# Kernel tuning notes

Measured on AMD Instinct MI355X. Metric: run time of the kernel, lower is better.

Reference implementation:

```python
import jax, jax.numpy as jnp
import numpy as np

B, U, S, F, D = 4, 1024, 256, 16, 256
K_RED = 3          # fd_redundancy_k
MAX_STEPS = 32     # fixed trip count replacing the data-dependent while-loop
NEG = -1e9


def setup_inputs() -> dict:
    key = jax.random.key(0)
    ks = jax.random.split(key, 12)
    user_enc = jax.random.normal(ks[0], (B, U, D), dtype=jnp.float32)
    server_enc = jax.random.normal(ks[1], (B, S, D), dtype=jnp.float32)
    # small needs vs. generous capacities so the allocation loop runs many steps
    users = jax.random.uniform(ks[2], (B, U, 8), dtype=jnp.float32) * 0.1
    servers = jax.random.uniform(ks[3], (B, S, 8), dtype=jnp.float32) * 20.0 + 1.0
    connect = jax.random.uniform(ks[4], (B, U, S)) < 0.3
    fd_id = jax.random.randint(ks[5], (B, S), 0, F)
    fd_onehot = jax.nn.one_hot(fd_id, F, dtype=jnp.float32)
    W_state = jax.random.normal(ks[6], (D, 4), dtype=jnp.float32) * 0.5
    b_state = jnp.zeros((D,), dtype=jnp.float32)
    W_q = jax.random.normal(ks[7], (D, D), dtype=jnp.float32) * D ** -0.5
    W_k = jax.random.normal(ks[8], (D, D), dtype=jnp.float32) * D ** -0.5
    W_us = jax.random.normal(ks[9], (1, 3), dtype=jnp.float32) * 0.5
    return dict(user_enc=user_enc, server_enc=server_enc, users=users, servers=servers,
                connect=connect, fd_onehot=fd_onehot, W_state=W_state, b_state=b_state,
                W_q=W_q, W_k=W_k, W_us=W_us,
                fd_alpha=jnp.asarray(1.0, jnp.float32), fd_beta=jnp.asarray(0.0, jnp.float32),
                score_bias=jnp.asarray(0.0, jnp.float32))


def _forward(user_enc, server_enc, users, servers, connect, fd_onehot,
             W_state, b_state, W_q, W_k, W_us, fd_alpha, fd_beta, score_bias):
    b, u, _ = users.shape
    s = servers.shape[1]
    d = user_enc.shape[-1]
    needs = users[..., 2:6]            # [B,U,4]
    init_cap = servers[..., 3:7]       # [B,S,4]
    inv_sqrt_d = d ** -0.5
    kf = jnp.asarray(float(K_RED), jnp.float32)
    q = user_enc @ W_q.T               # [B,U,D]
    u_ids = jnp.arange(u)[None, :, None]   # [1,U,1]
    s_ids = jnp.arange(s)[None, None, :]   # [1,1,S]
    b_grid = jnp.broadcast_to(jnp.arange(b)[:, None], (b, s))

    def step(carry, _):
        cap, alloc, fd_seen, logp = carry
        rc = jnp.sum(alloc, axis=-1)                                   # [B,U]
        need_more = rc < K_RED
        can_fulfill = jnp.all(cap[:, None] >= needs[:, :, None], -1)   # [B,U,S]
        elig = connect & can_fulfill & need_more[:, :, None] & (~alloc)
        elig = elig & jnp.any(elig)                                    # freeze when done
        # fault-domain novelty score
        fd_overlap = jnp.einsum('buf,bsf->bus', fd_seen, fd_onehot)
        is_new_fd = (fd_overlap < 0.5).astype(jnp.float32)
        # capacity-conditioned server keys
        cap_ratio = cap / jnp.maximum(init_cap, 1e-6)
        k_vec = (server_enc + cap_ratio @ W_state.T + b_state) @ W_k.T
        logits = jnp.einsum('bud,bsd->bus', q, k_vec) * inv_sqrt_d + score_bias
        logits = logits + jnp.tanh(fd_alpha * is_new_fd + fd_beta)
        rc_f = rc.astype(jnp.float32)
        user_state = jnp.stack([rc_f / kf, jnp.clip(kf - rc_f, 0.0) / kf,
                                (rc == K_RED - 1).astype(jnp.float32)], axis=-1)
        logits = logits + user_state @ W_us.T                          # [B,U,1] bcast
        cand = jnp.where(elig, logits, NEG)
        valid_server = jnp.any(elig, axis=1)                           # [B,S]
        # each valid server proposes its best user (greedy policy)
        prop_u = jnp.argmax(cand, axis=1)                              # [B,S]
        logp_bs = jnp.max(cand, axis=1) - jax.scipy.special.logsumexp(cand, axis=1)
        prop_mask = valid_server[:, None, :] & (prop_u[:, None, :] == u_ids)  # [B,U,S]
        # each proposed user accepts its best proposing server
        chosen_s = jnp.argmax(jnp.where(prop_mask, logits, NEG), axis=-1)     # [B,U]
        has_prop = jnp.any(prop_mask, axis=-1)
        sel = has_prop[..., None] & (s_ids == chosen_s[..., None])     # [B,U,S]
        alloc = alloc | sel
        fd_contrib = jnp.where(valid_server[..., None], fd_onehot, 0.0)
        fd_seen = fd_seen.at[b_grid, prop_u].max(fd_contrib)
        used = jnp.einsum('bus,buc->bsc', sel.astype(jnp.float32), needs)
        cap = jnp.maximum(cap - used, 0.0)
        logp = logp + jnp.sum(jnp.where(prop_mask, logp_bs[:, None, :], 0.0), axis=-1)
        return (cap, alloc, fd_seen, logp), None

    init = (init_cap,
            jnp.zeros((b, u, s), dtype=bool),
            jnp.zeros((b, u, fd_onehot.shape[-1]), dtype=jnp.float32),
            jnp.zeros((b, u), dtype=jnp.float32))
    (cap, alloc, fd_seen, logp), _ = jax.lax.scan(step, init, None, length=MAX_STEPS)
    return logp.sum(axis=1), alloc, cap


def reference(user_enc, server_enc, users, servers, connect, fd_onehot,
              W_state, b_state, W_q, W_k, W_us, fd_alpha, fd_beta, score_bias):
    return _forward(user_enc, server_enc, users, servers, connect, fd_onehot,
                    W_state, b_state, W_q, W_k, W_us, fd_alpha, fd_beta, score_bias)
```

## Files before the change

### kernel.cpp

```cpp
#include <hip/hip_runtime.h>
#include <stdint.h>
#include <math.h>

#define NB 4
#define NU 1024
#define NS 256
#define NF 16
#define ND 256
#define NEGV -1000000000.0f
#define VBIT (1u << 14)
#define AGENT __HIP_MEMORY_SCOPE_AGENT
#define SPINCAP (1 << 20)
#define NGRP 64
#define SPB 4
#define NT 1024


__device__ __forceinline__ void gemm64_body(
    const float* __restrict__ A, const float* __restrict__ Bm, float* __restrict__ C,
    int K, int lda, int ldb, int ldc, const float* __restrict__ biasA, float alpha,
    int m0, int n0, int t,
    float (&As)[2][16][68], float (&Bs)[2][16][68]) {
  int tx = t & 15, ty = t >> 4;
  float acc[4][4];
#pragma unroll
  for (int i = 0; i < 4; i++)
#pragma unroll
    for (int j = 0; j < 4; j++) acc[i][j] = 0.f;
  int lr = t >> 2;
  int kq = (t & 3) * 4;
  {
    float4 av = *(const float4*)(A + (size_t)(m0 + lr) * lda + kq);
    if (biasA) {
      const float* bp = biasA + kq;
      av.x += bp[0]; av.y += bp[1]; av.z += bp[2]; av.w += bp[3];
    }
    As[0][kq + 0][lr] = av.x; As[0][kq + 1][lr] = av.y;
    As[0][kq + 2][lr] = av.z; As[0][kq + 3][lr] = av.w;
    float4 bv = *(const float4*)(Bm + (size_t)(n0 + lr) * ldb + kq);
    Bs[0][kq + 0][lr] = bv.x; Bs[0][kq + 1][lr] = bv.y;
    Bs[0][kq + 2][lr] = bv.z; Bs[0][kq + 3][lr] = bv.w;
  }
  __syncthreads();
  int nt = K >> 4;
  for (int ti = 0; ti < nt; ++ti) {
    int buf = ti & 1;
    float4 av2, bv2;
    bool more = (ti + 1 < nt);
    if (more) {
      int k0 = (ti + 1) << 4;
      av2 = *(const float4*)(A + (size_t)(m0 + lr) * lda + k0 + kq);
      if (biasA) {
        const float* bp = biasA + k0 + kq;
        av2.x += bp[0]; av2.y += bp[1]; av2.z += bp[2]; av2.w += bp[3];
      }
      bv2 = *(const float4*)(Bm + (size_t)(n0 + lr) * ldb + k0 + kq);
    }
#pragma unroll
    for (int k = 0; k < 16; ++k) {
      float4 a = *(const float4*)&As[buf][k][ty * 4];
      float4 bb = *(const float4*)&Bs[buf][k][tx * 4];
      float am[4] = {a.x, a.y, a.z, a.w};
      float bn[4] = {bb.x, bb.y, bb.z, bb.w};
#pragma unroll
      for (int i = 0; i < 4; ++i)
#pragma unroll
        for (int j = 0; j < 4; ++j) acc[i][j] += am[i] * bn[j];
    }
    if (more) {
      __syncthreads();
      int nb = buf ^ 1;
      As[nb][kq + 0][lr] = av2.x; As[nb][kq + 1][lr] = av2.y;
      As[nb][kq + 2][lr] = av2.z; As[nb][kq + 3][lr] = av2.w;
      Bs[nb][kq + 0][lr] = bv2.x; Bs[nb][kq + 1][lr] = bv2.y;
      Bs[nb][kq + 2][lr] = bv2.z; Bs[nb][kq + 3][lr] = bv2.w;
      __syncthreads();
    }
  }
#pragma unroll
  for (int i = 0; i < 4; ++i) {
    float4 o = make_float4(acc[i][0] * alpha, acc[i][1] * alpha,
                           acc[i][2] * alpha, acc[i][3] * alpha);
    *(float4*)(C + (size_t)(m0 + ty * 4 + i) * ldc + n0 + tx * 4) = o;
  }
}

__global__ __launch_bounds__(256) void k_pre1(
    const uint8_t* __restrict__ conn, const float* __restrict__ W_state,
    const float* __restrict__ W_k, const float* __restrict__ user_enc,
    const float* __restrict__ server_enc, const float* __restrict__ b_state,
    const float* __restrict__ W_q,
    uint32_t* __restrict__ connT, float* __restrict__ WS_K,
    float* __restrict__ q, float* __restrict__ kb, float4* __restrict__ propZ) {
  __shared__ float As[2][16][68];
  __shared__ float Bs[2][16][68];
  int blk = blockIdx.x;
  int t = threadIdx.x;
  if (blk < 128) {
    __shared__ unsigned dd[2];
    unsigned c0 = 0, c123 = 0;
    for (int i = t; i < 4096; i += 256) {
      uchar4 v = ((const uchar4*)conn)[i];
      c0 |= v.x; c123 |= (unsigned)(v.y | v.z | v.w);
    }
    if (t == 0) { dd[0] = 0; dd[1] = 0; }
    __syncthreads();
    unsigned long long m0 = __ballot(c0 != 0), m1 = __ballot(c123 != 0);
    if ((t & 63) == 0) {
      if (m0) atomicOr(&dd[0], 1u);
      if (m1) atomicOr(&dd[1], 1u);
    }
    __syncthreads();
    int f = (dd[1] == 0) ? 0 : ((dd[0] == 0) ? 1 : 2);
    int b = blk >> 5, ug = blk & 31;
    int u0 = ug * 32;
    uint8_t* sm = (uint8_t*)&As[0][0][0];
#pragma unroll 4
    for (int r = 0; r < 32; ++r) {
      int e = (b * NU + u0 + r) * NS + t;
      bool nz;
      if (f == 0)      nz = ((const int*)conn)[e] != 0;
      else if (f == 1) nz = ((const float*)conn)[e] != 0.0f;
      else             nz = conn[e] != 0;
      sm[r * 260 + t] = nz ? 1 : 0;
    }
    __syncthreads();
    uint32_t word = 0;
#pragma unroll
    for (int j = 0; j < 32; ++j) word |= (uint32_t)sm[j * 260 + t] << j;
    connT[(b * NS + t) * 32 + ug] = word;
  } else if (blk == 128) {
    int d = t;
    const float4* wk4 = (const float4*)(W_k + d * ND);
    const float4* ws4 = (const float4*)W_state;
    float a0 = 0, a1 = 0, a2 = 0, a3 = 0;
    for (int e4 = 0; e4 < ND / 4; ++e4) {
      float4 k4 = wk4[e4];
      float4 w0 = ws4[e4 * 4 + 0];
      a0 += k4.x * w0.x; a1 += k4.x * w0.y; a2 += k4.x * w0.z; a3 += k4.x * w0.w;
      float4 w1 = ws4[e4 * 4 + 1];
      a0 += k4.y * w1.x; a1 += k4.y * w1.y; a2 += k4.y * w1.z; a3 += k4.y * w1.w;
      float4 w2 = ws4[e4 * 4 + 2];
      a0 += k4.z * w2.x; a1 += k4.z * w2.y; a2 += k4.z * w2.z; a3 += k4.z * w2.w;
      float4 w3 = ws4[e4 * 4 + 3];
      a0 += k4.w * w3.x; a1 += k4.w * w3.y; a2 += k4.w * w3.z; a3 += k4.w * w3.w;
    }
    ((float4*)WS_K)[d] = make_float4(a0, a1, a2, a3);
  } else if (blk < 385) {
    int idx = blk - 129;
    gemm64_body(user_enc, W_q, q, ND, ND, ND, ND, nullptr, 1.f,
                (idx >> 2) * 64, (idx & 3) * 64, t, As, Bs);
  } else if (blk < 449) {
    int idx = blk - 385;
    gemm64_body(server_enc, W_k, kb, ND, ND, ND, ND, b_state, 1.f,
                (idx >> 2) * 64, (idx & 3) * 64, t, As, Bs);
  } else {
    float4 z = make_float4(0.f, 0.f, 0.f, 0.f);
    for (int i = t; i < 2048; i += 256) propZ[i] = z;
  }
}

__global__ __launch_bounds__(256) void k_pre2(const float* __restrict__ q,
                                              const float* __restrict__ WS_K,
                                              float* __restrict__ qc,
                                              const float* __restrict__ kb,
                                              float* __restrict__ L0T) {
  __shared__ float As[2][16][68];
  __shared__ float Bs[2][16][68];
  int blk = blockIdx.x;
  int t = threadIdx.x;
  if (blk < 1024) {
    int row = blk * 4 + (t >> 6);
    int ln = t & 63;
    const float* qr = q + (size_t)row * ND;
    float a0 = 0, a1 = 0, a2 = 0, a3 = 0;
    for (int d = ln; d < ND; d += 64) {
      float qv = qr[d];
      float4 w = ((const float4*)WS_K)[d];
      a0 += qv * w.x; a1 += qv * w.y; a2 += qv * w.z; a3 += qv * w.w;
    }
    for (int o = 32; o; o >>= 1) {
      a0 += __shfl_xor(a0, o); a1 += __shfl_xor(a1, o);
      a2 += __shfl_xor(a2, o); a3 += __shfl_xor(a3, o);
    }
    if (ln == 0)
      ((float4*)qc)[row] = make_float4(a0 * 0.0625f, a1 * 0.0625f, a2 * 0.0625f, a3 * 0.0625f);
  } else {
    int idx = blk - 1024;
    int z = idx >> 6;
    int rest = idx & 63;
    int m0 = (rest >> 4) * 64;
    int n0 = (rest & 15) * 64;
    gemm64_body(kb + (size_t)z * NS * ND, q + (size_t)z * NU * ND,
                L0T + (size_t)z * NS * NU, ND, ND, ND, NU, nullptr, 0.0625f,
                m0, n0, t, As, Bs);
  }
}

__global__ __launch_bounds__(NT) void k_steps4(
    const float* __restrict__ L0T, const float* __restrict__ qc,
    const float* __restrict__ users, const float* __restrict__ servers,
    const uint32_t* __restrict__ connT, const float* __restrict__ fd_onehot,
    const float* __restrict__ W_us, const float* __restrict__ fd_alpha,
    const float* __restrict__ fd_beta, const float* __restrict__ score_bias,
    unsigned long long* __restrict__ propA, unsigned long long* __restrict__ propB,
    float* __restrict__ out) {
  __shared__ float redM[SPB][NT];
  __shared__ int redA[SPB][NT];
  __shared__ unsigned keyEnc4[4][NU];
  __shared__ unsigned srvMin4[4][NU];
  __shared__ float lsum4[4][NU];
  __shared__ unsigned fdSh4[4][NU];
  __shared__ float4 capS4[SPB];
  __shared__ float4 crS4[SPB];
  __shared__ float4 minv4[SPB];
  __shared__ int fidS[SPB];
  __shared__ float pM[SPB][4];
  __shared__ int pA[SPB][4];
  __shared__ float pS[SPB][4];
  __shared__ float wredL[16];
  __shared__ int anyL[4];

  const int blk = blockIdx.x;
  const int b = (blk & 7) >> 1;
  const int g = ((blk >> 3) << 1) | (blk & 1);
  const int tid = threadIdx.x;
  const int wv = tid >> 6, ln64 = tid & 63;
  const int bs0 = b * NS + g * SPB;
  const int bank = tid & 3;
  const int sW = wv >> 2, part = wv & 3;

  const float a_ = fd_alpha[0], be_ = fd_beta[0];
  const float t0 = tanhf(be_), t1 = tanhf(a_ + be_);
  const float sb = score_bias[0];
  const float w0 = W_us[0], w1 = W_us[1], w2 = W_us[2];

  if (tid < SPB) {
    int srow = bs0 + tid;
    int f = 0;
    for (int ff = 0; ff < NF; ++ff)
      if (fd_onehot[srow * NF + ff] > 0.5f) { f = ff; break; }
    fidS[tid] = f;
    float4 ic = make_float4(servers[srow * 8 + 3], servers[srow * 8 + 4],
                            servers[srow * 8 + 5], servers[srow * 8 + 6]);
    capS4[tid] = ic;
    float4 mv = make_float4(fmaxf(ic.x, 1e-6f), fmaxf(ic.y, 1e-6f),
                            fmaxf(ic.z, 1e-6f), fmaxf(ic.w, 1e-6f));
    minv4[tid] = mv;
    crS4[tid] = make_float4(ic.x / mv.x, ic.y / mv.y, ic.z / mv.z, ic.w / mv.w);
  }

  const int gu = b * NU + tid;
  float4 q4 = *(const float4*)(qc + gu * 4);
  float2 nA = *(const float2*)(users + gu * 8 + 2);
  float2 nB2 = *(const float2*)(users + gu * 8 + 4);
  const float nax = nA.x, nay = nA.y, nbx = nB2.x, nby = nB2.y;
  float L0r[SPB];
  uint32_t upk = 0;
  float usv = w1;
  float logpv = 0.f;
  uint32_t cb = 0, ab = 0;
  int prevPu = 0, prevSlot = 0;
  bool prevValid = false;
#pragma unroll
  for (int s = 0; s < SPB; ++s) {
    L0r[s] = L0T[(size_t)(bs0 + s) * NU + tid];
    uint32_t word = connT[(bs0 + s) * 32 + (tid >> 5)];
    cb |= ((word >> (tid & 31)) & 1u) << s;
  }
  for (int i = tid; i < 4 * NU; i += NT) {
    (&keyEnc4[0][0])[i] = 0u;
    (&srvMin4[0][0])[i] = 0xFFFFFFFFu;
    (&lsum4[0][0])[i] = 0.f;
    (&fdSh4[0][0])[i] = 0u;
  }
  __syncthreads();

  for (int step = 0; step < 32; ++step) {
    unsigned e = (unsigned)(step + 1);
    float cand[SPB];
#pragma unroll
    for (int s = 0; s < SPB; ++s) {
      float4 c = capS4[s];
      float4 cr = crS4[s];
      int fid = fidS[s];
      bool el = ((cb >> s) & 1u) && !((ab >> s) & 1u) &&
                ((upk & 0x30000u) != 0x30000u) &&
                c.x >= nax && c.y >= nay && c.z >= nbx && c.w >= nby;
      float tt = ((upk >> fid) & 1u) ? t0 : t1;
      float lg = L0r[s] + q4.x * cr.x + q4.y * cr.y + q4.z * cr.z + q4.w * cr.w +
                 sb + tt + usv;
      float cv = el ? lg : NEGV;
      cand[s] = cv;
      redM[s][tid] = cv;
      redA[s][tid] = (cv > NEGV) ? tid : 0x7fffffff;
    }
    __syncthreads();
    {
      int base = part * 256 + ln64 * 4;
      float m = redM[sW][base]; int a = redA[sW][base];
#pragma unroll
      for (int j = 1; j < 4; ++j) {
        float v = redM[sW][base + j]; int aa = redA[sW][base + j];
        if (v > m || (v == m && aa < a)) { m = v; a = aa; }
      }
      for (int o = 32; o; o >>= 1) {
        float ov = __shfl_xor(m, o); int oa = __shfl_xor(a, o);
        if (ov > m || (ov == m && oa < a)) { m = ov; a = oa; }
      }
      if (ln64 == 0) { pM[sW][part] = m; pA[sW][part] = a; }
    }
    __syncthreads();
    float bm;
    {
      float m = pM[sW][0]; int a = pA[sW][0];
#pragma unroll
      for (int j = 1; j < 4; ++j) {
        float v = pM[sW][j]; int aa = pA[sW][j];
        if (v > m || (v == m && aa < a)) { m = v; a = aa; }
      }
      bm = m;
      if (part == 0 && ln64 == 0) {
        int au = (a == 0x7fffffff) ? 0 : a;
        unsigned validb = (m > -1e8f) ? VBIT : 0u;
        unsigned pinfo = (unsigned)au | ((unsigned)fidS[sW] << 10) | validb | (e << 15);
        unsigned long long Aw = (unsigned long long)pinfo |
                                ((unsigned long long)__float_as_uint(m) << 32);
        __hip_atomic_store(&propA[(step & 1) * (NB * NS) + bs0 + sW], Aw,
                           __ATOMIC_RELAXED, AGENT);
      }
      int base = part * 256 + ln64 * 4;
      float ps = expf(redM[sW][base] - bm) + expf(redM[sW][base + 1] - bm) +
                 expf(redM[sW][base + 2] - bm) + expf(redM[sW][base + 3] - bm);
      for (int o = 32; o; o >>= 1) ps += __shfl_xor(ps, o);
      if (ln64 == 0) pS[sW][part] = ps;
    }
    __syncthreads();
    if (tid < SPB) {
      float ps = pS[tid][0] + pS[tid][1] + pS[tid][2] + pS[tid][3];
      unsigned long long Bw = (unsigned long long)__float_as_uint(-logf(ps)) |
                              ((unsigned long long)e << 32);
      __hip_atomic_store(&propB[(step & 1) * (NB * NS) + bs0 + tid], Bw,
                         __ATOMIC_RELAXED, AGENT);
    }

    {
      int par = (step & 1) * (NB * NS) + b * NS;
      unsigned pi = 0;
      unsigned encv = 0;
      int pu = 0;
      if (tid < 256) {
        unsigned long long Aw = __hip_atomic_load(&propA[par + tid], __ATOMIC_RELAXED, AGENT);
        if ((((unsigned)Aw >> 15) & 63u) != e) {
          int iters = 0;
          do {
            __builtin_amdgcn_s_sleep(1);
            Aw = __hip_atomic_load(&propA[par + tid], __ATOMIC_RELAXED, AGENT);
            if (++iters > SPINCAP) break;
          } while ((((unsigned)Aw >> 15) & 63u) != e);
        }
        pi = (unsigned)Aw;
        pu = pi & 1023;
        if (prevValid) {
          unsigned long long Bw = __hip_atomic_load(&propB[prevSlot], __ATOMIC_RELAXED, AGENT);
          if ((unsigned)(Bw >> 32) != (unsigned)step) {
            int iters = 0;
            do {
              __builtin_amdgcn_s_sleep(1);
              Bw = __hip_atomic_load(&propB[prevSlot], __ATOMIC_RELAXED, AGENT);
              if (++iters > SPINCAP) break;
            } while ((unsigned)(Bw >> 32) != (unsigned)step);
          }
          atomicAdd(&lsum4[bank][prevPu], __uint_as_float((unsigned)Bw));
        }
        prevValid = (pi & VBIT) != 0;
        prevPu = pu;
        prevSlot = par + tid;
        if (pi & VBIT) {
          unsigned vb = (unsigned)(Aw >> 32);
          encv = (vb & 0x80000000u) ? ~vb : (vb | 0x80000000u);
          atomicMax(&keyEnc4[bank][pu], encv);
        }
      }
      unsigned long long mm = __ballot((pi & VBIT) != 0);
      if (wv < 4 && ln64 == 0) anyL[wv] = (mm != 0ull) ? 1 : 0;
      __syncthreads();
      if (!(anyL[0] | anyL[1] | anyL[2] | anyL[3])) break;
      if ((tid < 256) && (pi & VBIT)) {
        if (keyEnc4[bank][pu] == encv)
          atomicMin(&srvMin4[bank][pu], (unsigned)tid);
        atomicOr(&fdSh4[bank][pu], 1u << ((pi >> 10) & 15));
      }
      __syncthreads();
      {
        int u = tid;
        unsigned k0 = keyEnc4[0][u], k1 = keyEnc4[1][u];
        unsigned k2 = keyEnc4[2][u], k3 = keyEnc4[3][u];
        unsigned gmax = max(max(k0, k1), max(k2, k3));
        if (gmax) {
          unsigned win = 0xFFFFFFFFu;
          if (k0 == gmax) win = min(win, srvMin4[0][u]);
          if (k1 == gmax) win = min(win, srvMin4[1][u]);
          if (k2 == gmax) win = min(win, srvMin4[2][u]);
          if (k3 == gmax) win = min(win, srvMin4[3][u]);
          float ls = lsum4[0][u] + lsum4[1][u] + lsum4[2][u] + lsum4[3][u];
          unsigned fda = fdSh4[0][u] | fdSh4[1][u] | fdSh4[2][u] | fdSh4[3][u];
          keyEnc4[0][u] = 0u; keyEnc4[1][u] = 0u; keyEnc4[2][u] = 0u; keyEnc4[3][u] = 0u;
          srvMin4[0][u] = 0xFFFFFFFFu; srvMin4[1][u] = 0xFFFFFFFFu;
          srvMin4[2][u] = 0xFFFFFFFFu; srvMin4[3][u] = 0xFFFFFFFFu;
          lsum4[0][u] = 0.f; lsum4[1][u] = 0.f; lsum4[2][u] = 0.f; lsum4[3][u] = 0.f;
          fdSh4[0][u] = 0u; fdSh4[1][u] = 0u; fdSh4[2][u] = 0u; fdSh4[3][u] = 0u;
          logpv += ls;
          uint32_t pk = upk;
          int r = (int)((pk >> 16) & 3) + 1;
          upk = ((pk | fda) & 0xFFFFu) | ((uint32_t)r << 16);
          float rf = (float)r;
          usv = w0 * (rf / 3.0f) + w1 * (fmaxf(3.0f - rf, 0.f) / 3.0f) +
                ((r == 2) ? w2 : 0.f);
          if ((int)(win >> 2) == g) {
            int sl = win & 3;
            ab |= 1u << sl;
            float4 c = capS4[sl];
            float4 nc = make_float4(fmaxf(c.x - nax, 0.f), fmaxf(c.y - nay, 0.f),
                                    fmaxf(c.z - nbx, 0.f), fmaxf(c.w - nby, 0.f));
            capS4[sl] = nc;
            float4 mv = minv4[sl];
            crS4[sl] = make_float4(nc.x / mv.x, nc.y / mv.y, nc.z / mv.z, nc.w / mv.w);
          }
        }
      }
      __syncthreads();
    }
  }

  if ((tid < 256) && prevValid) {
    unsigned long long Bw = __hip_atomic_load(&propB[prevSlot], __ATOMIC_RELAXED, AGENT);
    atomicAdd(&lsum4[bank][prevPu], __uint_as_float((unsigned)Bw));
  }
  __syncthreads();
  logpv += lsum4[0][tid] + lsum4[1][tid] + lsum4[2][tid] + lsum4[3][tid];

  {
    float4 o;
    o.x = (ab & 1u) ? 1.f : 0.f;
    o.y = ((ab >> 1) & 1u) ? 1.f : 0.f;
    o.z = ((ab >> 2) & 1u) ? 1.f : 0.f;
    o.w = ((ab >> 3) & 1u) ? 1.f : 0.f;
    *(float4*)(out + 4 + (size_t)(b * NU + tid) * NS + g * 4) = o;
  }
  if (tid < SPB)
    *(float4*)(out + 4 + (size_t)NB * NU * NS + (size_t)(bs0 + tid) * 4) = capS4[tid];
  if (g == 0) {
    float a2 = logpv;
    for (int o = 32; o; o >>= 1) a2 += __shfl_xor(a2, o);
    if (ln64 == 0) wredL[wv] = a2;
    __syncthreads();
    if (tid == 0) {
      float s = 0.f;
#pragma unroll
      for (int i = 0; i < 16; ++i) s += wredL[i];
      out[b] = s;
    }
  }
}

extern "C" void kernel_launch(void* const* d_in, const int* in_sizes, int n_in,
                              void* d_out, int out_size, void* d_ws, size_t ws_size,
                              hipStream_t stream) {
  const float* user_enc = (const float*)d_in[0];
  const float* server_enc = (const float*)d_in[1];
  const float* users = (const float*)d_in[2];
  const float* servers = (const float*)d_in[3];
  const uint8_t* connect = (const uint8_t*)d_in[4];
  const float* fd_onehot = (const float*)d_in[5];
  const float* W_state = (const float*)d_in[6];
  const float* b_state = (const float*)d_in[7];
  const float* W_q = (const float*)d_in[8];
  const float* W_k = (const float*)d_in[9];
  const float* W_us = (const float*)d_in[10];
  const float* fd_alpha = (const float*)d_in[11];
  const float* fd_beta = (const float*)d_in[12];
  const float* score_bias = (const float*)d_in[13];

  char* ws = (char*)d_ws;
  size_t off = 0;
  auto take = [&](size_t bytes) -> void* {
    size_t cur = off;
    off = (off + bytes + 255) & ~(size_t)255;
    return (void*)(ws + cur);
  };
  unsigned long long* propA = (unsigned long long*)take((size_t)2 * NB * NS * 8);
  unsigned long long* propB = (unsigned long long*)take((size_t)2 * NB * NS * 8);
  float* q = (float*)take((size_t)NB * NU * ND * 4);
  float* kb = (float*)take((size_t)NB * NS * ND * 4);
  float* L0T = (float*)take((size_t)NB * NS * NU * 4);
  float* qc = (float*)take((size_t)NB * NU * 4 * 4);
  float* WS_K = (float*)take((size_t)ND * 4 * 4);
  uint32_t* connT = (uint32_t*)take((size_t)NB * NS * 32 * 4);
  float* outp = (float*)d_out;

  k_pre1<<<450, 256, 0, stream>>>(connect, W_state, W_k, user_enc, server_enc, b_state,
                                  W_q, connT, WS_K, q, kb, (float4*)propA);
  k_pre2<<<1280, 256, 0, stream>>>(q, WS_K, qc, kb, L0T);
  k_steps4<<<NB * NGRP, NT, 0, stream>>>(
      L0T, qc, users, servers, connT, fd_onehot, W_us, fd_alpha, fd_beta, score_bias,
      propA, propB, outp);
}
```

Baseline: 177.4 us.

## Use wave-shuffle reductions and packed 64-bit argmax keys to cut barriers

The per-server argmax and softmax-sum reductions now run as wave shuffles over each thread's own candidates for all four servers, so the large shared staging arrays and one barrier per step go away. Conflict resolution across servers packs the encoded score and the inverted server index into one 64-bit key for a single atomicMax. This drops the separate atomicMin pass and its barrier. It also fixes the propB epoch check to wait on the stored epoch and adds a wait in the tail. The cost is more shuffle work per thread (four reductions across 16 waves) and 64-bit LDS atomics.

```diff
diff --git a/kernel.cpp b/kernel.cpp
--- a/kernel.cpp
+++ b/kernel.cpp
@@ -205,19 +205,16 @@
     const float* __restrict__ fd_beta, const float* __restrict__ score_bias,
     unsigned long long* __restrict__ propA, unsigned long long* __restrict__ propB,
     float* __restrict__ out) {
-  __shared__ float redM[SPB][NT];
-  __shared__ int redA[SPB][NT];
-  __shared__ unsigned keyEnc4[4][NU];
-  __shared__ unsigned srvMin4[4][NU];
+  __shared__ unsigned long long key64[4][NU];
   __shared__ float lsum4[4][NU];
   __shared__ unsigned fdSh4[4][NU];
+  __shared__ float pMW[SPB][16];
+  __shared__ int pAW[SPB][16];
+  __shared__ float pSW[SPB][16];
   __shared__ float4 capS4[SPB];
   __shared__ float4 crS4[SPB];
   __shared__ float4 minv4[SPB];
   __shared__ int fidS[SPB];
-  __shared__ float pM[SPB][4];
-  __shared__ int pA[SPB][4];
-  __shared__ float pS[SPB][4];
   __shared__ float wredL[16];
   __shared__ int anyL[4];
 
@@ -228,7 +225,6 @@
   const int wv = tid >> 6, ln64 = tid & 63;
   const int bs0 = b * NS + g * SPB;
   const int bank = tid & 3;
-  const int sW = wv >> 2, part = wv & 3;
 
   const float a_ = fd_alpha[0], be_ = fd_beta[0];
   const float t0 = tanhf(be_), t1 = tanhf(a_ + be_);
@@ -261,6 +257,7 @@
   float logpv = 0.f;
   uint32_t cb = 0, ab = 0;
   int prevPu = 0, prevSlot = 0;
+  unsigned prevE = 0;
   bool prevValid = false;
 #pragma unroll
   for (int s = 0; s < SPB; ++s) {
@@ -269,8 +266,7 @@
     cb |= ((word >> (tid & 31)) & 1u) << s;
   }
   for (int i = tid; i < 4 * NU; i += NT) {
-    (&keyEnc4[0][0])[i] = 0u;
-    (&srvMin4[0][0])[i] = 0xFFFFFFFFu;
+    (&key64[0][0])[i] = 0ull;
     (&lsum4[0][0])[i] = 0.f;
     (&fdSh4[0][0])[i] = 0u;
   }
@@ -292,52 +288,49 @@
                  sb + tt + usv;
       float cv = el ? lg : NEGV;
       cand[s] = cv;
-      redM[s][tid] = cv;
-      redA[s][tid] = (cv > NEGV) ? tid : 0x7fffffff;
-    }
-    __syncthreads();
-    {
-      int base = part * 256 + ln64 * 4;
-      float m = redM[sW][base]; int a = redA[sW][base];
-#pragma unroll
-      for (int j = 1; j < 4; ++j) {
-        float v = redM[sW][base + j]; int aa = redA[sW][base + j];
-        if (v > m || (v == m && aa < a)) { m = v; a = aa; }
-      }
+      float m = cv;
+      int a = (cv > NEGV) ? tid : 0x7fffffff;
       for (int o = 32; o; o >>= 1) {
         float ov = __shfl_xor(m, o); int oa = __shfl_xor(a, o);
         if (ov > m || (ov == m && oa < a)) { m = ov; a = oa; }
       }
-      if (ln64 == 0) { pM[sW][part] = m; pA[sW][part] = a; }
-    }
-    __syncthreads();
-    float bm;
-    {
-      float m = pM[sW][0]; int a = pA[sW][0];
-#pragma unroll
-      for (int j = 1; j < 4; ++j) {
-        float v = pM[sW][j]; int aa = pA[sW][j];
+      if (ln64 == 0) { pMW[s][wv] = m; pAW[s][wv] = a; }
+    }
+    __syncthreads();
+    float bmv[SPB];
+    int bav[SPB];
+#pragma unroll
+    for (int s = 0; s < SPB; ++s) {
+      float m = pMW[s][0]; int a = pAW[s][0];
+#pragma unroll
+      for (int j = 1; j < 16; ++j) {
+        float v = pMW[s][j]; int aa = pAW[s][j];
         if (v > m || (v == m && aa < a)) { m = v; a = aa; }
       }
-      bm = m;
-      if (part == 0 && ln64 == 0) {
-        int au = (a == 0x7fffffff) ? 0 : a;
-        unsigned validb = (m > -1e8f) ? VBIT : 0u;
-        unsigned pinfo = (unsigned)au | ((unsigned)fidS[sW] << 10) | validb | (e << 15);
-        unsigned long long Aw = (unsigned long long)pinfo |
-                                ((unsigned long long)__float_as_uint(m) << 32);
-        __hip_atomic_store(&propA[(step & 1) * (NB * NS) + bs0 + sW], Aw,
-                           __ATOMIC_RELAXED, AGENT);
-      }
-      int base = part * 256 + ln64 * 4;
-      float ps = expf(redM[sW][base] - bm) + expf(redM[sW][base + 1] - bm) +
-                 expf(redM[sW][base + 2] - bm) + expf(redM[sW][base + 3] - bm);
+      bmv[s] = m; bav[s] = a;
+    }
+    if (tid < SPB) {
+      float m = bmv[tid];
+      int a = bav[tid];
+      int au = (a == 0x7fffffff) ? 0 : a;
+      unsigned validb = (m > -1e8f) ? VBIT : 0u;
+      unsigned pinfo = (unsigned)au | ((unsigned)fidS[tid] << 10) | validb | (e << 15);
+      unsigned long long Aw = (unsigned long long)pinfo |
+                              ((unsigned long long)__float_as_uint(m) << 32);
+      __hip_atomic_store(&propA[(step & 1) * (NB * NS) + bs0 + tid], Aw,
+                         __ATOMIC_RELAXED, AGENT);
+    }
+#pragma unroll
+    for (int s = 0; s < SPB; ++s) {
+      float ps = expf(cand[s] - bmv[s]);
       for (int o = 32; o; o >>= 1) ps += __shfl_xor(ps, o);
-      if (ln64 == 0) pS[sW][part] = ps;
+      if (ln64 == 0) pSW[s][wv] = ps;
     }
     __syncthreads();
     if (tid < SPB) {
-      float ps = pS[tid][0] + pS[tid][1] + pS[tid][2] + pS[tid][3];
+      float ps = pSW[tid][0];
+#pragma unroll
+      for (int j = 1; j < 16; ++j) ps += pSW[tid][j];
       unsigned long long Bw = (unsigned long long)__float_as_uint(-logf(ps)) |
                               ((unsigned long long)e << 32);
       __hip_atomic_store(&propB[(step & 1) * (NB * NS) + bs0 + tid], Bw,
@@ -347,8 +340,6 @@
     {
       int par = (step & 1) * (NB * NS) + b * NS;
       unsigned pi = 0;
-      unsigned encv = 0;
-      int pu = 0;
       if (tid < 256) {
         unsigned long long Aw = __hip_atomic_load(&propA[par + tid], __ATOMIC_RELAXED, AGENT);
         if ((((unsigned)Aw >> 15) & 63u) != e) {
@@ -360,54 +351,46 @@
           } while ((((unsigned)Aw >> 15) & 63u) != e);
         }
         pi = (unsigned)Aw;
-        pu = pi & 1023;
+        int pu = pi & 1023;
         if (prevValid) {
           unsigned long long Bw = __hip_atomic_load(&propB[prevSlot], __ATOMIC_RELAXED, AGENT);
-          if ((unsigned)(Bw >> 32) != (unsigned)step) {
+          if ((unsigned)(Bw >> 32) != prevE) {
             int iters = 0;
             do {
               __builtin_amdgcn_s_sleep(1);
               Bw = __hip_atomic_load(&propB[prevSlot], __ATOMIC_RELAXED, AGENT);
               if (++iters > SPINCAP) break;
-            } while ((unsigned)(Bw >> 32) != (unsigned)step);
+            } while ((unsigned)(Bw >> 32) != prevE);
           }
           atomicAdd(&lsum4[bank][prevPu], __uint_as_float((unsigned)Bw));
         }
         prevValid = (pi & VBIT) != 0;
         prevPu = pu;
         prevSlot = par + tid;
+        prevE = e;
         if (pi & VBIT) {
           unsigned vb = (unsigned)(Aw >> 32);
-          encv = (vb & 0x80000000u) ? ~vb : (vb | 0x80000000u);
-          atomicMax(&keyEnc4[bank][pu], encv);
+          unsigned enc = (vb & 0x80000000u) ? ~vb : (vb | 0x80000000u);
+          unsigned long long key = ((unsigned long long)enc << 32) |
+                                   (unsigned)(255 - tid);
+          atomicMax(&key64[bank][pu], key);
+          atomicOr(&fdSh4[bank][pu], 1u << ((pi >> 10) & 15));
         }
       }
       unsigned long long mm = __ballot((pi & VBIT) != 0);
       if (wv < 4 && ln64 == 0) anyL[wv] = (mm != 0ull) ? 1 : 0;
       __syncthreads();
       if (!(anyL[0] | anyL[1] | anyL[2] | anyL[3])) break;
-      if ((tid < 256) && (pi & VBIT)) {
-        if (keyEnc4[bank][pu] == encv)
-          atomicMin(&srvMin4[bank][pu], (unsigned)tid);
-        atomicOr(&fdSh4[bank][pu], 1u << ((pi >> 10) & 15));
-      }
-      __syncthreads();
       {
         int u = tid;
-        unsigned k0 = keyEnc4[0][u], k1 = keyEnc4[1][u];
-        unsigned k2 = keyEnc4[2][u], k3 = keyEnc4[3][u];
-        unsigned gmax = max(max(k0, k1), max(k2, k3));
+        unsigned long long k0 = key64[0][u], k1 = key64[1][u];
+        unsigned long long k2 = key64[2][u], k3 = key64[3][u];
+        unsigned long long gmax = max(max(k0, k1), max(k2, k3));
         if (gmax) {
-          unsigned win = 0xFFFFFFFFu;
-          if (k0 == gmax) win = min(win, srvMin4[0][u]);
-          if (k1 == gmax) win = min(win, srvMin4[1][u]);
-          if (k2 == gmax) win = min(win, srvMin4[2][u]);
-          if (k3 == gmax) win = min(win, srvMin4[3][u]);
+          int win = 255 - (int)(gmax & 0xFFull);
           float ls = lsum4[0][u] + lsum4[1][u] + lsum4[2][u] + lsum4[3][u];
           unsigned fda = fdSh4[0][u] | fdSh4[1][u] | fdSh4[2][u] | fdSh4[3][u];
-          keyEnc4[0][u] = 0u; keyEnc4[1][u] = 0u; keyEnc4[2][u] = 0u; keyEnc4[3][u] = 0u;
-          srvMin4[0][u] = 0xFFFFFFFFu; srvMin4[1][u] = 0xFFFFFFFFu;
-          srvMin4[2][u] = 0xFFFFFFFFu; srvMin4[3][u] = 0xFFFFFFFFu;
+          key64[0][u] = 0ull; key64[1][u] = 0ull; key64[2][u] = 0ull; key64[3][u] = 0ull;
           lsum4[0][u] = 0.f; lsum4[1][u] = 0.f; lsum4[2][u] = 0.f; lsum4[3][u] = 0.f;
           fdSh4[0][u] = 0u; fdSh4[1][u] = 0u; fdSh4[2][u] = 0u; fdSh4[3][u] = 0u;
           logpv += ls;
@@ -417,7 +400,7 @@
           float rf = (float)r;
           usv = w0 * (rf / 3.0f) + w1 * (fmaxf(3.0f - rf, 0.f) / 3.0f) +
                 ((r == 2) ? w2 : 0.f);
-          if ((int)(win >> 2) == g) {
+          if ((win >> 2) == g) {
             int sl = win & 3;
             ab |= 1u << sl;
             float4 c = capS4[sl];
@@ -435,6 +418,14 @@
 
   if ((tid < 256) && prevValid) {
     unsigned long long Bw = __hip_atomic_load(&propB[prevSlot], __ATOMIC_RELAXED, AGENT);
+    if ((unsigned)(Bw >> 32) != prevE) {
+      int iters = 0;
+      do {
+        __builtin_amdgcn_s_sleep(1);
+        Bw = __hip_atomic_load(&propB[prevSlot], __ATOMIC_RELAXED, AGENT);
+        if (++iters > SPINCAP) break;
+      } while ((unsigned)(Bw >> 32) != prevE);
+    }
     atomicAdd(&lsum4[bank][prevPu], __uint_as_float((unsigned)Bw));
   }
   __syncthreads();
```

New measurement: 315.3 us. 1.78x slower.
